# Kernel tuning notes

Measured on AMD Instinct MI355X. Metric: run time of the kernel, lower is better.

## Reference

```python
import jax, jax.numpy as jnp
import numpy as np

D_MODEL, N_HEADS, D_K = 768, 12, 64
LN_EPS = 1e-5


def setup_inputs() -> dict:
    key = jax.random.key(0)
    ks = jax.random.split(key, 8)
    b, c, n, s = 8, 32, 4, 64
    scale = 1.0 / np.sqrt(D_MODEL)
    inp = {
        "e": jax.random.normal(ks[0], (b, c, n, s, D_MODEL), dtype=jnp.float32),
        "h": jax.random.normal(ks[1], (b, c, s, D_MODEL), dtype=jnp.float32),
        # weights stored [in, out] (torch Linear transposed)
        "Wq": jax.random.normal(ks[2], (D_MODEL, N_HEADS * D_K), dtype=jnp.float32) * scale,
        "bq": jnp.zeros((N_HEADS * D_K,), dtype=jnp.float32),
        "Wk": jax.random.normal(ks[3], (D_MODEL, N_HEADS * D_K), dtype=jnp.float32) * scale,
        "bk": jnp.zeros((N_HEADS * D_K,), dtype=jnp.float32),
        "Wv": jax.random.normal(ks[4], (D_MODEL, N_HEADS * D_K), dtype=jnp.float32) * scale,
        "bv": jnp.zeros((N_HEADS * D_K,), dtype=jnp.float32),
        "Wo": jax.random.normal(ks[5], (N_HEADS * D_K, D_MODEL), dtype=jnp.float32) * scale,
        "bo": jnp.zeros((D_MODEL,), dtype=jnp.float32),
        "ln_g": jnp.ones((D_MODEL,), dtype=jnp.float32),
        "ln_b": jnp.zeros((D_MODEL,), dtype=jnp.float32),
    }
    return inp


def _layer_norm(x, g, b):
    mu = jnp.mean(x, axis=-1, keepdims=True)
    var = jnp.mean(jnp.square(x - mu), axis=-1, keepdims=True)
    return (x - mu) * jax.lax.rsqrt(var + LN_EPS) * g + b


def reference(e, h, Wq, bq, Wk, bk, Wv, bv, Wo, bo, ln_g, ln_b):
    # e: [b, c, n, i, d]  h: [b, c, j, d]
    e_res = e
    en = _layer_norm(e, ln_g, ln_b)
    b, c, n, i, _ = e.shape
    j = h.shape[2]
    q = (en @ Wq + bq).reshape(b, c, n, i, N_HEADS, D_K)
    k = (h @ Wk + bk).reshape(b, c, j, N_HEADS, D_K)
    v = (h @ Wv + bv).reshape(b, c, j, N_HEADS, D_K)
    attn = jnp.einsum('bcnihd,bcjhd->bcnhij', q, k) * (1.0 / np.sqrt(D_K))
    attn = jax.nn.softmax(attn, axis=-1)
    o = jnp.einsum('bcnhij,bcjhd->bcnihd', attn, v).reshape(b, c, n, i, N_HEADS * D_K)
    return o @ Wo + bo + e_res
```

## Files before the change

kernel.cpp:

```cpp
#include <hip/hip_runtime.h>

typedef __bf16 bf16x8 __attribute__((ext_vector_type(8)));
typedef __bf16 bf16x4 __attribute__((ext_vector_type(4)));
typedef float f32x4 __attribute__((ext_vector_type(4)));

__device__ __forceinline__ f32x4 mfma16(bf16x8 a, bf16x8 b, f32x4 c) {
  return __builtin_amdgcn_mfma_f32_16x16x32_bf16(a, b, c, 0, 0, 0);
}

__device__ __forceinline__ void load_lds16(const void* g, void* l) {
  __builtin_amdgcn_global_load_lds(
      (const __attribute__((address_space(1))) void*)g,
      (__attribute__((address_space(3))) void*)l, 16, 0, 0);
}

template <int NWG>
__device__ __forceinline__ int xcd_swz(int orig) {
  constexpr int NX = 8;
  constexpr int q = NWG / NX;
  constexpr int r = NWG % NX;
  const int xcd = orig % NX;
  const int pos = orig / NX;
  if constexpr (r == 0) {
    return xcd * q + pos;
  } else {
    return (xcd < r ? xcd * (q + 1) : r * (q + 1) + (xcd - r) * q) + pos;
  }
}

__global__ __launch_bounds__(256) void prep_ln_cast_kernel(
    const float* __restrict__ Wq, const float* __restrict__ Wk,
    const float* __restrict__ Wv, const float* __restrict__ Wo,
    __bf16* __restrict__ WqT, __bf16* __restrict__ WkvT, __bf16* __restrict__ WoT,
    const float* __restrict__ e, const float* __restrict__ gam,
    const float* __restrict__ bet, __bf16* __restrict__ en,
    const float* __restrict__ hin, __bf16* __restrict__ h_bf) {
  const int bid = blockIdx.x;
  const int t = threadIdx.x;
  if (bid < 2304) {
    __shared__ float tile[32][33];
    const int z = bid / 576;
    const int rr = bid % 576;
    const int bx = rr % 24, by = rr / 24;
    const float* W = (z == 0) ? Wq : (z == 1) ? Wk : (z == 2) ? Wv : Wo;
    __bf16* out = (z == 0) ? WqT : (z == 3) ? WoT : WkvT;
    const int rowOff = (z == 2) ? 768 : 0;
    const int tx = t & 31, ty = t >> 5;
    const int x = bx * 32 + tx;
    const int y = by * 32 + ty;
#pragma unroll
    for (int i = 0; i < 32; i += 8) tile[ty + i][tx] = W[(size_t)(y + i) * 768 + x];
    __syncthreads();
    const int nx = by * 32 + tx;
    const int ny = bx * 32 + ty;
#pragma unroll
    for (int i = 0; i < 32; i += 8)
      out[(size_t)(rowOff + ny + i) * 768 + nx] = (__bf16)tile[tx][ty + i];
  } else if (bid < 2304 + 16384) {
    const int lane = t & 63;
    const int wid = t >> 6;
    const size_t row = (size_t)(bid - 2304) * 4 + wid;
    const float* p = e + row * 768;
    float x[12];
    float sum = 0.f;
#pragma unroll
    for (int s = 0; s < 3; ++s) {
      f32x4 v = *(const f32x4*)(p + (s * 64 + lane) * 4);
#pragma unroll
      for (int q = 0; q < 4; ++q) { x[s * 4 + q] = v[q]; sum += v[q]; }
    }
#pragma unroll
    for (int d = 1; d < 64; d <<= 1) sum += __shfl_xor(sum, d);
    const float m = sum * (1.f / 768.f);
    float vs = 0.f;
#pragma unroll
    for (int q = 0; q < 12; ++q) { float d = x[q] - m; vs += d * d; }
#pragma unroll
    for (int d = 1; d < 64; d <<= 1) vs += __shfl_xor(vs, d);
    const float rr = rsqrtf(vs * (1.f / 768.f) + 1e-5f);
    __bf16* o = en + row * 768;
#pragma unroll
    for (int s = 0; s < 3; ++s) {
      f32x4 g4 = *(const f32x4*)(gam + (s * 64 + lane) * 4);
      f32x4 b4 = *(const f32x4*)(bet + (s * 64 + lane) * 4);
      bf16x4 pk;
#pragma unroll
      for (int q = 0; q < 4; ++q) pk[q] = (__bf16)((x[s * 4 + q] - m) * rr * g4[q] + b4[q]);
      *(bf16x4*)(o + (s * 64 + lane) * 4) = pk;
    }
  } else {
    constexpr int n4 = 16384 * 768 / 4;
    int i = (bid - 2304 - 16384) * 256 + t;
    for (; i < n4; i += 2048 * 256) {
      f32x4 v = ((const f32x4*)hin)[i];
      bf16x4 o;
#pragma unroll
      for (int q = 0; q < 4; ++q) o[q] = (__bf16)v[q];
      ((bf16x4*)h_bf)[i] = o;
    }
  }
}

enum { MODE_Q = 0, MODE_KV = 1, MODE_O = 2 };

template <int MODE, int NC>
__device__ __forceinline__ void gemm8_body(
    int wgid, __bf16* As, __bf16* Bs,
    const __bf16* __restrict__ A, const __bf16* __restrict__ WT,
    const float* __restrict__ bias0, const float* __restrict__ bias1,
    const float* __restrict__ eres,
    __bf16* __restrict__ dst0, __bf16* __restrict__ dst1,
    float* __restrict__ outp) {
  const int rowBase = (wgid / NC) * 256;
  const int colBase = (wgid % NC) * 256;
  const int t = threadIdx.x;
  const int lane = t & 63, wid = t >> 6;
  const int wm = wid >> 2, wn = wid & 3;
  const int lr = lane & 15, lg = lane >> 4;
  const int srow = t >> 2;
  const int skcol = ((t & 3) ^ (srow & 3)) * 8;
  const int cg = lg ^ (lr & 3);
  f32x4 acc[8][4] = {};

  auto stageA = [&](int kt) {
    const int slot = kt & 3;
#pragma unroll
    for (int p = 0; p < 2; ++p) {
      const int rowIn = p * 128 + srow;
      const __bf16* ga;
      if constexpr (MODE == MODE_O) {
        const int r = rowBase + rowIn;
        ga = A + ((((size_t)(r >> 6)) * 12 + (kt >> 1)) << 12) + ((r & 63) << 6) +
             (kt & 1) * 32 + skcol;
      } else {
        ga = A + (size_t)(rowBase + rowIn) * 768 + kt * 32 + skcol;
      }
      load_lds16(ga, &As[slot * 8192 + p * 4096 + t * 8]);
    }
  };
  auto stageB = [&](int kt) {
    const int slot = kt & 3;
#pragma unroll
    for (int p = 0; p < 2; ++p) {
      const int rowIn = p * 128 + srow;
      const __bf16* gb = WT + (size_t)(colBase + rowIn) * 768 + kt * 32 + skcol;
      load_lds16(gb, &Bs[slot * 8192 + p * 4096 + t * 8]);
    }
  };

  stageA(0); stageB(0);
  stageA(1); stageB(1);
  stageA(2); stageB(2);

#pragma unroll
  for (int kt = 0; kt < 24; ++kt) {
    const int slot = kt & 3;
    if (kt <= 21) {
      asm volatile("s_waitcnt vmcnt(8)" ::: "memory");
    } else if (kt == 22) {
      asm volatile("s_waitcnt vmcnt(4)" ::: "memory");
    } else {
      asm volatile("s_waitcnt vmcnt(0)" ::: "memory");
    }
    __builtin_amdgcn_sched_barrier(0);
    __builtin_amdgcn_s_barrier();

    bf16x8 b[4], a0[4];
#pragma unroll
    for (int it = 0; it < 4; ++it)
      a0[it] = *(const bf16x8*)&As[slot * 8192 + (wm * 128 + it * 16 + lr) * 32 + cg * 8];
#pragma unroll
    for (int jt = 0; jt < 4; ++jt)
      b[jt] = *(const bf16x8*)&Bs[slot * 8192 + (wn * 64 + jt * 16 + lr) * 32 + cg * 8];
    if (kt + 3 < 24) stageA(kt + 3);
    asm volatile("s_waitcnt lgkmcnt(0)" ::: "memory");
    __builtin_amdgcn_sched_barrier(0);
    __builtin_amdgcn_s_setprio(1);
#pragma unroll
    for (int it = 0; it < 4; ++it)
#pragma unroll
      for (int jt = 0; jt < 4; ++jt)
        acc[it][jt] = mfma16(a0[it], b[jt], acc[it][jt]);
    __builtin_amdgcn_s_setprio(0);
    __builtin_amdgcn_s_barrier();

    bf16x8 a1[4];
#pragma unroll
    for (int it = 0; it < 4; ++it)
      a1[it] = *(const bf16x8*)&As[slot * 8192 + (wm * 128 + (it + 4) * 16 + lr) * 32 + cg * 8];
    if (kt + 3 < 24) stageB(kt + 3);
    asm volatile("s_waitcnt lgkmcnt(0)" ::: "memory");
    __builtin_amdgcn_sched_barrier(0);
    __builtin_amdgcn_s_setprio(1);
#pragma unroll
    for (int it = 0; it < 4; ++it)
#pragma unroll
      for (int jt = 0; jt < 4; ++jt)
        acc[it + 4][jt] = mfma16(a1[it], b[jt], acc[it + 4][jt]);
    __builtin_amdgcn_s_setprio(0);
  }

  const int roww = rowBase + wm * 128;
  const int colw = colBase + wn * 64;
#pragma unroll
  for (int it = 0; it < 8; ++it) {
#pragma unroll
    for (int jt = 0; jt < 4; ++jt) {
      const int c = colw + jt * 16 + lr;
#pragma unroll
      for (int rg = 0; rg < 4; ++rg) {
        const int r = roww + it * 16 + lg * 4 + rg;
        const float val = acc[it][jt][rg];
        if constexpr (MODE == MODE_O) {
          outp[(size_t)r * 768 + c] = val + bias0[c] + eres[(size_t)r * 768 + c];
        } else if constexpr (MODE == MODE_Q) {
          dst0[((((size_t)(r >> 6)) * 12 + (c >> 6)) << 12) + ((r & 63) << 6) + (c & 63)] =
              (__bf16)(val + bias0[c]);
        } else {
          if (c < 768) {
            dst0[((((size_t)(r >> 6)) * 12 + (c >> 6)) << 12) + ((r & 63) << 6) + (c & 63)] =
                (__bf16)(val + bias0[c]);
          } else {
            const int c2 = c - 768;
            dst1[((((size_t)(r >> 6)) * 12 + (c2 >> 6)) << 12) + ((c2 & 63) << 6) + (r & 63)] =
                (__bf16)(val + bias1[c2]);
          }
        }
      }
    }
  }
}

__global__ __launch_bounds__(512) void gemm_qkv_kernel(
    const __bf16* __restrict__ en, const __bf16* __restrict__ WqT,
    const float* __restrict__ bq, __bf16* __restrict__ q_ws,
    const __bf16* __restrict__ h_bf, const __bf16* __restrict__ WkvT,
    const float* __restrict__ bk, const float* __restrict__ bv,
    __bf16* __restrict__ k_ws, __bf16* __restrict__ v_ws) {
  __shared__ __bf16 As[4 * 8192];
  __shared__ __bf16 Bs[4 * 8192];
  const int bid = blockIdx.x;
  if (bid < 768) {
    gemm8_body<MODE_Q, 3>(xcd_swz<768>(bid), As, Bs, en, WqT, bq, nullptr,
                          nullptr, q_ws, nullptr, nullptr);
  } else {
    gemm8_body<MODE_KV, 6>(xcd_swz<384>(bid - 768), As, Bs, h_bf, WkvT, bk, bv,
                           nullptr, k_ws, v_ws, nullptr);
  }
}

__global__ __launch_bounds__(512) void gemm_o_kernel(
    const __bf16* __restrict__ o_ws, const __bf16* __restrict__ WoT,
    const float* __restrict__ bo, const float* __restrict__ e,
    float* __restrict__ outp) {
  __shared__ __bf16 As[4 * 8192];
  __shared__ __bf16 Bs[4 * 8192];
  gemm8_body<MODE_O, 3>(xcd_swz<768>(blockIdx.x), As, Bs, o_ws, WoT, bo,
                        nullptr, e, nullptr, nullptr, outp);
}

__global__ __launch_bounds__(256) void attn_kernel(
    const __bf16* __restrict__ q, const __bf16* __restrict__ k,
    const __bf16* __restrict__ v, __bf16* __restrict__ o) {
  const int bh = blockIdx.x;
  const int h = bh % 12;
  const int bc = bh / 12;
  const int t = threadIdx.x;
  const int wid = t >> 6, lane = t & 63;
  const int lr = lane & 15, lg = lane >> 4;
  __shared__ __bf16 kL[64][72];
  __shared__ __bf16 vL[64][72];
  __shared__ __bf16 P[4][64][72];

  {
    const __bf16* kp = k + ((size_t)bh << 12);
    const __bf16* vp = v + ((size_t)bh << 12);
    const int row = t >> 2, col = (t & 3) * 16;
    *(bf16x8*)&kL[row][col]     = *(const bf16x8*)(kp + row * 64 + col);
    *(bf16x8*)&kL[row][col + 8] = *(const bf16x8*)(kp + row * 64 + col + 8);
    *(bf16x8*)&vL[row][col]     = *(const bf16x8*)(vp + row * 64 + col);
    *(bf16x8*)&vL[row][col + 8] = *(const bf16x8*)(vp + row * 64 + col + 8);
  }
  const __bf16* qp = q + (((size_t)(bc * 4 + wid) * 12 + h) << 12);
  __bf16* op = o + (((size_t)(bc * 4 + wid) * 12 + h) << 12);
  bf16x8 qf[4][2];
#pragma unroll
  for (int it = 0; it < 4; ++it)
#pragma unroll
    for (int kc = 0; kc < 2; ++kc)
      qf[it][kc] = *(const bf16x8*)(qp + (it * 16 + lr) * 64 + kc * 32 + lg * 8);
  __syncthreads();

  f32x4 s[4][4] = {};
#pragma unroll
  for (int kc = 0; kc < 2; ++kc) {
    bf16x8 kf[4];
#pragma unroll
    for (int jt = 0; jt < 4; ++jt)
      kf[jt] = *(const bf16x8*)&kL[jt * 16 + lr][kc * 32 + lg * 8];
#pragma unroll
    for (int jt = 0; jt < 4; ++jt)
#pragma unroll
      for (int it = 0; it < 4; ++it)
        s[jt][it] = mfma16(kf[jt], qf[it][kc], s[jt][it]);
  }

  float recip[4];
#pragma unroll
  for (int it = 0; it < 4; ++it) {
    float m = -1e30f;
#pragma unroll
    for (int jt = 0; jt < 4; ++jt)
#pragma unroll
      for (int rg = 0; rg < 4; ++rg) m = fmaxf(m, s[jt][it][rg]);
    m = fmaxf(m, __shfl_xor(m, 16));
    m = fmaxf(m, __shfl_xor(m, 32));
    float sum = 0.f;
#pragma unroll
    for (int jt = 0; jt < 4; ++jt) {
      bf16x4 pk;
#pragma unroll
      for (int rg = 0; rg < 4; ++rg) {
        float p = __expf((s[jt][it][rg] - m) * 0.125f);
        sum += p;
        pk[rg] = (__bf16)p;
      }
      *(bf16x4*)&P[wid][it * 16 + lr][jt * 16 + lg * 4] = pk;
    }
    sum += __shfl_xor(sum, 16);
    sum += __shfl_xor(sum, 32);
    recip[it] = 1.f / sum;
  }

  f32x4 oacc[4][4] = {};
#pragma unroll
  for (int kc = 0; kc < 2; ++kc) {
    bf16x8 vf[4], pf[4];
#pragma unroll
    for (int dt = 0; dt < 4; ++dt)
      vf[dt] = *(const bf16x8*)&vL[dt * 16 + lr][kc * 32 + lg * 8];
#pragma unroll
    for (int it = 0; it < 4; ++it)
      pf[it] = *(const bf16x8*)&P[wid][it * 16 + lr][kc * 32 + lg * 8];
#pragma unroll
    for (int dt = 0; dt < 4; ++dt)
#pragma unroll
      for (int it = 0; it < 4; ++it)
        oacc[dt][it] = mfma16(vf[dt], pf[it], oacc[dt][it]);
  }
#pragma unroll
  for (int it = 0; it < 4; ++it) {
    const float rc = recip[it];
#pragma unroll
    for (int dt = 0; dt < 4; ++dt) {
      bf16x4 pk;
#pragma unroll
      for (int rg = 0; rg < 4; ++rg) pk[rg] = (__bf16)(oacc[dt][it][rg] * rc);
      *(bf16x4*)(op + (size_t)(it * 16 + lr) * 64 + dt * 16 + lg * 4) = pk;
    }
  }
}

extern "C" void kernel_launch(void* const* d_in, const int* in_sizes, int n_in,
                              void* d_out, int out_size, void* d_ws, size_t ws_size,
                              hipStream_t stream) {
  const float* e  = (const float*)d_in[0];
  const float* h  = (const float*)d_in[1];
  const float* Wq = (const float*)d_in[2];
  const float* bq = (const float*)d_in[3];
  const float* Wk = (const float*)d_in[4];
  const float* bk = (const float*)d_in[5];
  const float* Wv = (const float*)d_in[6];
  const float* bv = (const float*)d_in[7];
  const float* Wo = (const float*)d_in[8];
  const float* bo = (const float*)d_in[9];
  const float* g  = (const float*)d_in[10];
  const float* b  = (const float*)d_in[11];
  float* outp = (float*)d_out;
  char* ws = (char*)d_ws;

  __bf16* WqT  = (__bf16*)(ws);
  __bf16* WkvT = (__bf16*)(ws + 1179648);
  __bf16* WoT  = (__bf16*)(ws + 3538944);
  char* R1 = ws + 4718592;
  __bf16* en    = (__bf16*)(R1);
  __bf16* k_ws  = (__bf16*)(R1 + 25165824);
  __bf16* v_ws  = (__bf16*)(R1 + 50331648);
  __bf16* q_ws  = (__bf16*)(ws + 105381888);
  __bf16* h_bf  = (__bf16*)(ws + 206045184);
  k_ws = (__bf16*)(ws + 231211008);
  v_ws = (__bf16*)(ws + 256376832);

  prep_ln_cast_kernel<<<2304 + 16384 + 2048, 256, 0, stream>>>(
      Wq, Wk, Wv, Wo, WqT, WkvT, WoT, e, g, b, en, h, h_bf);
  gemm_qkv_kernel<<<1152, 512, 0, stream>>>(
      en, WqT, bq, q_ws, h_bf, WkvT, bk, bv, k_ws, v_ws);
  attn_kernel<<<3072, 256, 0, stream>>>(q_ws, k_ws, v_ws, q_ws);
  gemm_o_kernel<<<768, 512, 0, stream>>>(q_ws, WoT, bo, e, outp);
}
```

Measured before the change: 453.5 us.

## Fuse LayerNorm and fp32-to-bf16 casts into QKV GEMM A-operand loading

The prep kernel now computes only per-row LayerNorm mean and rstd, folds gamma into Wq and beta into a new Q bias (bq2 = bq + beta·Wq). The QKV GEMM reads fp32 e and h directly through registers, normalizes and casts to bf16, then writes LDS, replacing the async global-to-LDS loads of pre-cast bf16 tensors. This removes writing and re-reading the bf16 en and h_bf buffers. In exchange the A loads go through VGPRs with extra waitcnts, the B prefetch depth drops, and A-side global traffic doubles because fp32 is read instead of bf16.

```diff
diff --git a/kernel.cpp b/kernel.cpp
--- a/kernel.cpp
+++ b/kernel.cpp
@@ -28,13 +28,13 @@
   }
 }
 
-__global__ __launch_bounds__(256) void prep_ln_cast_kernel(
+__global__ __launch_bounds__(256) void prep_kernel(
     const float* __restrict__ Wq, const float* __restrict__ Wk,
     const float* __restrict__ Wv, const float* __restrict__ Wo,
     __bf16* __restrict__ WqT, __bf16* __restrict__ WkvT, __bf16* __restrict__ WoT,
     const float* __restrict__ e, const float* __restrict__ gam,
-    const float* __restrict__ bet, __bf16* __restrict__ en,
-    const float* __restrict__ hin, __bf16* __restrict__ h_bf) {
+    const float* __restrict__ bet, float2* __restrict__ stats,
+    const float* __restrict__ bq, float* __restrict__ bq2) {
   const int bid = blockIdx.x;
   const int t = threadIdx.x;
   if (bid < 2304) {
@@ -49,17 +49,26 @@
     const int x = bx * 32 + tx;
     const int y = by * 32 + ty;
 #pragma unroll
-    for (int i = 0; i < 32; i += 8) tile[ty + i][tx] = W[(size_t)(y + i) * 768 + x];
+    for (int i = 0; i < 32; i += 8) {
+      float v = W[(size_t)(y + i) * 768 + x];
+      if (z == 0) v *= gam[y + i];
+      tile[ty + i][tx] = v;
+    }
     __syncthreads();
     const int nx = by * 32 + tx;
     const int ny = bx * 32 + ty;
 #pragma unroll
     for (int i = 0; i < 32; i += 8)
       out[(size_t)(rowOff + ny + i) * 768 + nx] = (__bf16)tile[tx][ty + i];
-  } else if (bid < 2304 + 16384) {
+  } else if (bid < 2307) {
+    const int n = (bid - 2304) * 256 + t;
+    float s = bq[n];
+    for (int k = 0; k < 768; ++k) s += bet[k] * Wq[(size_t)k * 768 + n];
+    bq2[n] = s;
+  } else {
     const int lane = t & 63;
     const int wid = t >> 6;
-    const size_t row = (size_t)(bid - 2304) * 4 + wid;
+    const size_t row = (size_t)(bid - 2307) * 4 + wid;
     const float* p = e + row * 768;
     float x[12];
     float sum = 0.f;
@@ -77,26 +86,11 @@
     for (int q = 0; q < 12; ++q) { float d = x[q] - m; vs += d * d; }
 #pragma unroll
     for (int d = 1; d < 64; d <<= 1) vs += __shfl_xor(vs, d);
-    const float rr = rsqrtf(vs * (1.f / 768.f) + 1e-5f);
-    __bf16* o = en + row * 768;
-#pragma unroll
-    for (int s = 0; s < 3; ++s) {
-      f32x4 g4 = *(const f32x4*)(gam + (s * 64 + lane) * 4);
-      f32x4 b4 = *(const f32x4*)(bet + (s * 64 + lane) * 4);
-      bf16x4 pk;
-#pragma unroll
-      for (int q = 0; q < 4; ++q) pk[q] = (__bf16)((x[s * 4 + q] - m) * rr * g4[q] + b4[q]);
-      *(bf16x4*)(o + (s * 64 + lane) * 4) = pk;
-    }
-  } else {
-    constexpr int n4 = 16384 * 768 / 4;
-    int i = (bid - 2304 - 16384) * 256 + t;
-    for (; i < n4; i += 2048 * 256) {
-      f32x4 v = ((const f32x4*)hin)[i];
-      bf16x4 o;
-#pragma unroll
-      for (int q = 0; q < 4; ++q) o[q] = (__bf16)v[q];
-      ((bf16x4*)h_bf)[i] = o;
+    if (lane == 0) {
+      float2 st;
+      st.x = m;
+      st.y = rsqrtf(vs * (1.f / 768.f) + 1e-5f);
+      stats[row] = st;
     }
   }
 }
@@ -104,13 +98,13 @@
 enum { MODE_Q = 0, MODE_KV = 1, MODE_O = 2 };
 
 template <int MODE, int NC>
-__device__ __forceinline__ void gemm8_body(
+__device__ __forceinline__ void gemm_f32a_body(
     int wgid, __bf16* As, __bf16* Bs,
-    const __bf16* __restrict__ A, const __bf16* __restrict__ WT,
+    const float* __restrict__ Afp, const float2* __restrict__ stats,
+    const __bf16* __restrict__ WT,
     const float* __restrict__ bias0, const float* __restrict__ bias1,
-    const float* __restrict__ eres,
-    __bf16* __restrict__ dst0, __bf16* __restrict__ dst1,
-    float* __restrict__ outp) {
+    __bf16* __restrict__ dst0, __bf16* __restrict__ dst1) {
+  constexpr int LA = (MODE == MODE_Q) ? 6 : 4;
   const int rowBase = (wgid / NC) * 256;
   const int colBase = (wgid % NC) * 256;
   const int t = threadIdx.x;
@@ -121,22 +115,36 @@
   const int skcol = ((t & 3) ^ (srow & 3)) * 8;
   const int cg = lg ^ (lr & 3);
   f32x4 acc[8][4] = {};
-
-  auto stageA = [&](int kt) {
+  f32x4 ra0, ra1, rb0, rb1;
+  float2 st0, st1;
+
+  auto loadA = [&](int kt) {
+    const float* g0 = Afp + (size_t)(rowBase + srow) * 768 + kt * 32 + skcol;
+    const float* g1 = Afp + (size_t)(rowBase + 128 + srow) * 768 + kt * 32 + skcol;
+    ra0 = *(const f32x4*)g0;
+    ra1 = *(const f32x4*)(g0 + 4);
+    rb0 = *(const f32x4*)g1;
+    rb1 = *(const f32x4*)(g1 + 4);
+    if constexpr (MODE == MODE_Q) {
+      st0 = stats[rowBase + srow];
+      st1 = stats[rowBase + 128 + srow];
+    }
+  };
+  auto writeA = [&](int kt) {
     const int slot = kt & 3;
-#pragma unroll
-    for (int p = 0; p < 2; ++p) {
-      const int rowIn = p * 128 + srow;
-      const __bf16* ga;
-      if constexpr (MODE == MODE_O) {
-        const int r = rowBase + rowIn;
-        ga = A + ((((size_t)(r >> 6)) * 12 + (kt >> 1)) << 12) + ((r & 63) << 6) +
-             (kt & 1) * 32 + skcol;
-      } else {
-        ga = A + (size_t)(rowBase + rowIn) * 768 + kt * 32 + skcol;
+    bf16x8 pk0, pk1;
+#pragma unroll
+    for (int j = 0; j < 4; ++j) {
+      float v0 = ra0[j], v1 = ra1[j], w0 = rb0[j], w1 = rb1[j];
+      if constexpr (MODE == MODE_Q) {
+        v0 = (v0 - st0.x) * st0.y; v1 = (v1 - st0.x) * st0.y;
+        w0 = (w0 - st1.x) * st1.y; w1 = (w1 - st1.x) * st1.y;
       }
-      load_lds16(ga, &As[slot * 8192 + p * 4096 + t * 8]);
-    }
+      pk0[j] = (__bf16)v0; pk0[j + 4] = (__bf16)v1;
+      pk1[j] = (__bf16)w0; pk1[j + 4] = (__bf16)w1;
+    }
+    *(bf16x8*)&As[slot * 8192 + t * 8] = pk0;
+    *(bf16x8*)&As[slot * 8192 + 4096 + t * 8] = pk1;
   };
   auto stageB = [&](int kt) {
     const int slot = kt & 3;
@@ -148,23 +156,42 @@
     }
   };
 
-  stageA(0); stageB(0);
-  stageA(1); stageB(1);
-  stageA(2); stageB(2);
+  stageB(0); stageB(1);
+  loadA(0);
+  asm volatile("s_waitcnt vmcnt(0)" ::: "memory");
+  __builtin_amdgcn_sched_barrier(0);
+  writeA(0);
+  loadA(1);
+  asm volatile("s_waitcnt vmcnt(0)" ::: "memory");
+  __builtin_amdgcn_sched_barrier(0);
+  writeA(1);
+  loadA(2);
+  asm volatile("s_waitcnt lgkmcnt(0)" ::: "memory");
+  __builtin_amdgcn_sched_barrier(0);
 
 #pragma unroll
   for (int kt = 0; kt < 24; ++kt) {
     const int slot = kt & 3;
-    if (kt <= 21) {
-      asm volatile("s_waitcnt vmcnt(8)" ::: "memory");
+    if (kt >= 2 && kt <= 21) {
+      asm volatile("s_waitcnt vmcnt(%0)" :: "i"(LA + 2) : "memory");
     } else if (kt == 22) {
-      asm volatile("s_waitcnt vmcnt(4)" ::: "memory");
-    } else {
+      asm volatile("s_waitcnt vmcnt(2)" ::: "memory");
+    } else if (kt == 23) {
       asm volatile("s_waitcnt vmcnt(0)" ::: "memory");
     }
     __builtin_amdgcn_sched_barrier(0);
     __builtin_amdgcn_s_barrier();
 
+    if (kt + 2 < 24) {
+      if (kt == 0) {
+        asm volatile("s_waitcnt vmcnt(0)" ::: "memory");
+      } else {
+        asm volatile("s_waitcnt vmcnt(2)" ::: "memory");
+      }
+      __builtin_amdgcn_sched_barrier(0);
+      writeA(kt + 2);
+    }
+    if (kt + 3 < 24) loadA(kt + 3);
     bf16x8 b[4], a0[4];
 #pragma unroll
     for (int it = 0; it < 4; ++it)
@@ -172,7 +199,6 @@
 #pragma unroll
     for (int jt = 0; jt < 4; ++jt)
       b[jt] = *(const bf16x8*)&Bs[slot * 8192 + (wn * 64 + jt * 16 + lr) * 32 + cg * 8];
-    if (kt + 3 < 24) stageA(kt + 3);
     asm volatile("s_waitcnt lgkmcnt(0)" ::: "memory");
     __builtin_amdgcn_sched_barrier(0);
     __builtin_amdgcn_s_setprio(1);
@@ -188,7 +214,7 @@
 #pragma unroll
     for (int it = 0; it < 4; ++it)
       a1[it] = *(const bf16x8*)&As[slot * 8192 + (wm * 128 + (it + 4) * 16 + lr) * 32 + cg * 8];
-    if (kt + 3 < 24) stageB(kt + 3);
+    if (kt + 2 < 24) stageB(kt + 2);
     asm volatile("s_waitcnt lgkmcnt(0)" ::: "memory");
     __builtin_amdgcn_sched_barrier(0);
     __builtin_amdgcn_s_setprio(1);
@@ -211,9 +237,7 @@
       for (int rg = 0; rg < 4; ++rg) {
         const int r = roww + it * 16 + lg * 4 + rg;
         const float val = acc[it][jt][rg];
-        if constexpr (MODE == MODE_O) {
-          outp[(size_t)r * 768 + c] = val + bias0[c] + eres[(size_t)r * 768 + c];
-        } else if constexpr (MODE == MODE_Q) {
+        if constexpr (MODE == MODE_Q) {
           dst0[((((size_t)(r >> 6)) * 12 + (c >> 6)) << 12) + ((r & 63) << 6) + (c & 63)] =
               (__bf16)(val + bias0[c]);
         } else {
@@ -231,21 +255,128 @@
   }
 }
 
+template <int NC>
+__device__ __forceinline__ void gemm_o_body(
+    int wgid, __bf16* As, __bf16* Bs,
+    const __bf16* __restrict__ A, const __bf16* __restrict__ WT,
+    const float* __restrict__ bias0, const float* __restrict__ eres,
+    float* __restrict__ outp) {
+  const int rowBase = (wgid / NC) * 256;
+  const int colBase = (wgid % NC) * 256;
+  const int t = threadIdx.x;
+  const int lane = t & 63, wid = t >> 6;
+  const int wm = wid >> 2, wn = wid & 3;
+  const int lr = lane & 15, lg = lane >> 4;
+  const int srow = t >> 2;
+  const int skcol = ((t & 3) ^ (srow & 3)) * 8;
+  const int cg = lg ^ (lr & 3);
+  f32x4 acc[8][4] = {};
+
+  auto stageA = [&](int kt) {
+    const int slot = kt & 3;
+#pragma unroll
+    for (int p = 0; p < 2; ++p) {
+      const int rowIn = p * 128 + srow;
+      const int r = rowBase + rowIn;
+      const __bf16* ga = A + ((((size_t)(r >> 6)) * 12 + (kt >> 1)) << 12) + ((r & 63) << 6) +
+                         (kt & 1) * 32 + skcol;
+      load_lds16(ga, &As[slot * 8192 + p * 4096 + t * 8]);
+    }
+  };
+  auto stageB = [&](int kt) {
+    const int slot = kt & 3;
+#pragma unroll
+    for (int p = 0; p < 2; ++p) {
+      const int rowIn = p * 128 + srow;
+      const __bf16* gb = WT + (size_t)(colBase + rowIn) * 768 + kt * 32 + skcol;
+      load_lds16(gb, &Bs[slot * 8192 + p * 4096 + t * 8]);
+    }
+  };
+
+  stageA(0); stageB(0);
+  stageA(1); stageB(1);
+  stageA(2); stageB(2);
+
+#pragma unroll
+  for (int kt = 0; kt < 24; ++kt) {
+    const int slot = kt & 3;
+    if (kt <= 21) {
+      asm volatile("s_waitcnt vmcnt(8)" ::: "memory");
+    } else if (kt == 22) {
+      asm volatile("s_waitcnt vmcnt(4)" ::: "memory");
+    } else {
+      asm volatile("s_waitcnt vmcnt(0)" ::: "memory");
+    }
+    __builtin_amdgcn_sched_barrier(0);
+    __builtin_amdgcn_s_barrier();
+
+    bf16x8 b[4], a0[4];
+#pragma unroll
+    for (int it = 0; it < 4; ++it)
+      a0[it] = *(const bf16x8*)&As[slot * 8192 + (wm * 128 + it * 16 + lr) * 32 + cg * 8];
+#pragma unroll
+    for (int jt = 0; jt < 4; ++jt)
+      b[jt] = *(const bf16x8*)&Bs[slot * 8192 + (wn * 64 + jt * 16 + lr) * 32 + cg * 8];
+    if (kt + 3 < 24) stageA(kt + 3);
+    asm volatile("s_waitcnt lgkmcnt(0)" ::: "memory");
+    __builtin_amdgcn_sched_barrier(0);
+    __builtin_amdgcn_s_setprio(1);
+#pragma unroll
+    for (int it = 0; it < 4; ++it)
+#pragma unroll
+      for (int jt = 0; jt < 4; ++jt)
+        acc[it][jt] = mfma16(a0[it], b[jt], acc[it][jt]);
+    __builtin_amdgcn_s_setprio(0);
+    __builtin_amdgcn_s_barrier();
+
+    bf16x8 a1[4];
+#pragma unroll
+    for (int it = 0; it < 4; ++it)
+      a1[it] = *(const bf16x8*)&As[slot * 8192 + (wm * 128 + (it + 4) * 16 + lr) * 32 + cg * 8];
+    if (kt + 3 < 24) stageB(kt + 3);
+    asm volatile("s_waitcnt lgkmcnt(0)" ::: "memory");
+    __builtin_amdgcn_sched_barrier(0);
+    __builtin_amdgcn_s_setprio(1);
+#pragma unroll
+    for (int it = 0; it < 4; ++it)
+#pragma unroll
+      for (int jt = 0; jt < 4; ++jt)
+        acc[it + 4][jt] = mfma16(a1[it], b[jt], acc[it + 4][jt]);
+    __builtin_amdgcn_s_setprio(0);
+  }
+
+  const int roww = rowBase + wm * 128;
+  const int colw = colBase + wn * 64;
+#pragma unroll
+  for (int it = 0; it < 8; ++it) {
+#pragma unroll
+    for (int jt = 0; jt < 4; ++jt) {
+      const int c = colw + jt * 16 + lr;
+#pragma unroll
+      for (int rg = 0; rg < 4; ++rg) {
+        const int r = roww + it * 16 + lg * 4 + rg;
+        outp[(size_t)r * 768 + c] = acc[it][jt][rg] + bias0[c] + eres[(size_t)r * 768 + c];
+      }
+    }
+  }
+}
+
 __global__ __launch_bounds__(512) void gemm_qkv_kernel(
-    const __bf16* __restrict__ en, const __bf16* __restrict__ WqT,
-    const float* __restrict__ bq, __bf16* __restrict__ q_ws,
-    const __bf16* __restrict__ h_bf, const __bf16* __restrict__ WkvT,
+    const float* __restrict__ e, const float2* __restrict__ stats,
+    const __bf16* __restrict__ WqT, const float* __restrict__ bq2,
+    __bf16* __restrict__ q_ws,
+    const float* __restrict__ h, const __bf16* __restrict__ WkvT,
     const float* __restrict__ bk, const float* __restrict__ bv,
     __bf16* __restrict__ k_ws, __bf16* __restrict__ v_ws) {
   __shared__ __bf16 As[4 * 8192];
   __shared__ __bf16 Bs[4 * 8192];
   const int bid = blockIdx.x;
   if (bid < 768) {
-    gemm8_body<MODE_Q, 3>(xcd_swz<768>(bid), As, Bs, en, WqT, bq, nullptr,
-                          nullptr, q_ws, nullptr, nullptr);
+    gemm_f32a_body<MODE_Q, 3>(xcd_swz<768>(bid), As, Bs, e, stats, WqT, bq2,
+                              nullptr, q_ws, nullptr);
   } else {
-    gemm8_body<MODE_KV, 6>(xcd_swz<384>(bid - 768), As, Bs, h_bf, WkvT, bk, bv,
-                           nullptr, k_ws, v_ws, nullptr);
+    gemm_f32a_body<MODE_KV, 6>(xcd_swz<384>(bid - 768), As, Bs, h, nullptr,
+                               WkvT, bk, bv, k_ws, v_ws);
   }
 }
 
@@ -255,8 +386,7 @@
     float* __restrict__ outp) {
   __shared__ __bf16 As[4 * 8192];
   __shared__ __bf16 Bs[4 * 8192];
-  gemm8_body<MODE_O, 3>(xcd_swz<768>(blockIdx.x), As, Bs, o_ws, WoT, bo,
-                        nullptr, e, nullptr, nullptr, outp);
+  gemm_o_body<3>(xcd_swz<768>(blockIdx.x), As, Bs, o_ws, WoT, bo, e, outp);
 }
 
 __global__ __launch_bounds__(256) void attn_kernel(
@@ -379,22 +509,19 @@
   float* outp = (float*)d_out;
   char* ws = (char*)d_ws;
 
-  __bf16* WqT  = (__bf16*)(ws);
-  __bf16* WkvT = (__bf16*)(ws + 1179648);
-  __bf16* WoT  = (__bf16*)(ws + 3538944);
-  char* R1 = ws + 4718592;
-  __bf16* en    = (__bf16*)(R1);
-  __bf16* k_ws  = (__bf16*)(R1 + 25165824);
-  __bf16* v_ws  = (__bf16*)(R1 + 50331648);
-  __bf16* q_ws  = (__bf16*)(ws + 105381888);
-  __bf16* h_bf  = (__bf16*)(ws + 206045184);
-  k_ws = (__bf16*)(ws + 231211008);
-  v_ws = (__bf16*)(ws + 256376832);
-
-  prep_ln_cast_kernel<<<2304 + 16384 + 2048, 256, 0, stream>>>(
-      Wq, Wk, Wv, Wo, WqT, WkvT, WoT, e, g, b, en, h, h_bf);
+  __bf16* WqT   = (__bf16*)(ws);
+  __bf16* WkvT  = (__bf16*)(ws + 1179648);
+  __bf16* WoT   = (__bf16*)(ws + 3538944);
+  float2* stats = (float2*)(ws + 4718592);
+  float*  bq2   = (float*)(ws + 5242880);
+  __bf16* k_ws  = (__bf16*)(ws + 8388608);
+  __bf16* v_ws  = (__bf16*)(ws + 33554432);
+  __bf16* q_ws  = (__bf16*)(ws + 58720256);
+
+  prep_kernel<<<2307 + 16384, 256, 0, stream>>>(
+      Wq, Wk, Wv, Wo, WqT, WkvT, WoT, e, g, b, stats, bq, bq2);
   gemm_qkv_kernel<<<1152, 512, 0, stream>>>(
-      en, WqT, bq, q_ws, h_bf, WkvT, bk, bv, k_ws, v_ws);
+      e, stats, WqT, bq2, q_ws, h, WkvT, bk, bv, k_ws, v_ws);
   attn_kernel<<<3072, 256, 0, stream>>>(q_ws, k_ws, v_ws, q_ws);
   gemm_o_kernel<<<768, 512, 0, stream>>>(q_ws, WoT, bo, e, outp);
 }
```

Measured after the change: 489.1 us. 7.8% more time.
